# Kernel optimization log

Measured on AMD Instinct MI355X. Metric: run time of the kernel, lower is better.

Reference implementation:

```python
import jax, jax.numpy as jnp
import numpy as np

STRIDE = 1
PADDING = 1
DILATION = 1


def setup_inputs() -> dict:
    key = jax.random.key(0)
    k1, k2 = jax.random.split(key)
    N, C_in, H, W = 32, 128, 56, 56
    C_out, ksz = 256, 3
    x = jax.random.normal(k1, (N, C_in, H, W), dtype=jnp.float32)
    # xavier_normal_ with gain sqrt(2): std = gain*sqrt(2/(fan_in+fan_out))
    fan_in = C_in * ksz * ksz
    fan_out = C_out * ksz * ksz
    std = np.sqrt(2.0) * np.sqrt(2.0 / (fan_in + fan_out))
    weight = jax.random.normal(k2, (C_out, C_in, ksz, ksz), dtype=jnp.float32) * jnp.float32(std)
    bias = jnp.zeros((C_out,), dtype=jnp.float32)
    return {"x": x, "weight": weight, "bias": bias}


def reference(x, weight, bias):
    # Faithful to conv2d(X, K, stride, padding, dilation, bias):
    # unfold (im2col) + matmul + fold is mathematically a standard cross-correlation
    # conv; expressed here with the efficient lax primitive.
    y = jax.lax.conv_general_dilated(
        x, weight,
        window_strides=(STRIDE, STRIDE),
        padding=[(PADDING, PADDING), (PADDING, PADDING)],
        rhs_dilation=(DILATION, DILATION),
        dimension_numbers=("NCHW", "OIHW", "NCHW"),
    )
    return y + bias[None, :, None, None]
```

## Files before the change

kernel.cpp:

```cpp
#include <hip/hip_runtime.h>
#include <hip/hip_bf16.h>


#define CIN   128
#define HH    56
#define WW    56
#define COUT  256
#define HW    3136
#define NIMG  32
#define NP    (NIMG * HW)
#define XPW   58
#define XPIX  (XPW * XPW)
#define XPAD_BYTES (NIMG * XPIX * CIN * 2)
#define WT_OFF     XPAD_BYTES

typedef __bf16 bf16x8 __attribute__((ext_vector_type(8)));
typedef float  f32x4  __attribute__((ext_vector_type(4)));

#define GLD16(g, l) __builtin_amdgcn_global_load_lds( \
    (const __attribute__((address_space(1))) void*)(g), \
    (__attribute__((address_space(3))) void*)(l), 16, 0, 0)

__device__ __forceinline__ unsigned pack_bf16(float a, float b) {
    return (__float_as_uint(b) & 0xFFFF0000u) | (__float_as_uint(a) >> 16);
}

__global__ __launch_bounds__(128) void prep_x(const float* __restrict__ x,
                                              __hip_bfloat16* __restrict__ xp) {
    __shared__ unsigned short t[HH * CIN];
    const int b  = blockIdx.x;
    const int n  = b / HH;
    const int y  = b - n * HH;
    const int ci = threadIdx.x;

    const float* src = x + ((size_t)(n * CIN + ci) * HW) + y * WW;
    #pragma unroll
    for (int j = 0; j < 14; ++j) {
        const float4 v = ((const float4*)src)[j];
        t[(4 * j + 0) * CIN + ci] = (unsigned short)(__float_as_uint(v.x) >> 16);
        t[(4 * j + 1) * CIN + ci] = (unsigned short)(__float_as_uint(v.y) >> 16);
        t[(4 * j + 2) * CIN + ci] = (unsigned short)(__float_as_uint(v.z) >> 16);
        t[(4 * j + 3) * CIN + ci] = (unsigned short)(__float_as_uint(v.w) >> 16);
    }

    const uint4 z = make_uint4(0, 0, 0, 0);
    if (ci < 32) {
        const int side = ci >> 4;
        const int j    = ci & 15;
        ((uint4*)(xp + ((size_t)n * XPIX + (y + 1) * XPW + side * 57) * CIN))[j] = z;
    }
    if (y == 0)
        for (int j = ci; j < 928; j += 128)
            ((uint4*)(xp + (size_t)n * XPIX * CIN))[j] = z;
    if (y == HH - 1)
        for (int j = ci; j < 928; j += 128)
            ((uint4*)(xp + ((size_t)n * XPIX + 57 * XPW) * CIN))[j] = z;

    __syncthreads();

    uint4* dst = (uint4*)(xp + ((size_t)n * XPIX + (y + 1) * XPW + 1) * CIN);
    const uint4* lsrc = (const uint4*)t;
    #pragma unroll
    for (int j = 0; j < 7; ++j)
        dst[j * 128 + ci] = lsrc[j * 128 + ci];
}

__global__ __launch_bounds__(256) void prep_w(const float* __restrict__ w,
                                              __hip_bfloat16* __restrict__ wt) {
    const int co = blockIdx.x * 2 + (threadIdx.x >> 7);
    const int ci = threadIdx.x & 127;
    const float* src = w + (size_t)(co * CIN + ci) * 9;
    #pragma unroll
    for (int tp = 0; tp < 9; ++tp)
        wt[(size_t)tp * (COUT * CIN) + co * CIN + ci] = __float2bfloat16(src[tp]);
}

__global__ __launch_bounds__(256) void conv_main(
    const char* __restrict__ xpb,
    const char* __restrict__ wtb,
    const float* __restrict__ bias,
    float* __restrict__ out)
{
    __shared__ __align__(16) char L[65536];

    const int tid  = threadIdx.x;
    const int l    = tid & 63;
    const int wv   = tid >> 6;
    const int wm   = wv & 1;
    const int wn   = wv >> 1;
    const int l15  = l & 15;
    const int quad = l >> 4;

    const int idx = blockIdx.x;
    const int bm  = (idx >> 3) & 1;
    const int bn  = (idx >> 4) * 8 + (idx & 7);
    const int pbase  = bn * 128;
    const int cobase = bm * 128;

    const int gseg = (l & 3) ^ ((l >> 3) & 3);
    unsigned aoff[2], boff[2];
    #pragma unroll
    for (int j = 0; j < 2; ++j) {
        const int c   = wv * 2 + j;
        const int row = c * 16 + (l >> 2);
        aoff[j] = (unsigned)((cobase + row) * 256 + gseg * 16);
        const int p   = pbase + row;
        const int n   = p / HW;
        const int rem = p - n * HW;
        const int y   = rem / WW;
        const int x   = rem - y * WW;
        boff[j] = (unsigned)((n * XPIX + y * XPW + x) * 256 + gseg * 16);
    }
    const int segoff = (quad ^ ((l15 >> 1) & 3)) << 4;

    f32x4 acc[4][4];
    #pragma unroll
    for (int i = 0; i < 4; ++i)
        #pragma unroll
        for (int j = 0; j < 4; ++j)
            acc[i][j] = (f32x4){0.f, 0.f, 0.f, 0.f};

    auto STAGE = [&](int s, int bufw) {
        const int t  = s >> 2;
        const int kq = s & 3;
        const int r  = t / 3;
        const int sx = t - 3 * r;
        const unsigned wo = (unsigned)(t * (COUT * CIN * 2) + kq * 64);
        const unsigned bo = (unsigned)((r * XPW + sx) * 256 + kq * 64);
        char* Ab = L + bufw * 8192;
        char* Bb = L + 32768 + bufw * 8192;
        #pragma unroll
        for (int j = 0; j < 2; ++j) {
            const int c = wv * 2 + j;
            GLD16(wtb + wo + aoff[j], Ab + c * 1024);
            GLD16(xpb + bo + boff[j], Bb + c * 1024);
        }
    };

    STAGE(0, 0);
    STAGE(1, 1);
    STAGE(2, 2);

    #pragma unroll
    for (int s = 0; s < 36; ++s) {
        asm volatile("s_waitcnt vmcnt(8)" ::: "memory");
        __builtin_amdgcn_s_barrier();
        asm volatile("" ::: "memory");

        STAGE((s + 3 < 36) ? s + 3 : 35, (s + 3) & 3);

        const char* Ab = L + (s & 3) * 8192;
        const char* Bb = L + 32768 + (s & 3) * 8192;
        bf16x8 af[4], bfr[4];
        #pragma unroll
        for (int mt = 0; mt < 4; ++mt)
            af[mt] = *(const bf16x8*)(Ab + (wm * 64 + mt * 16 + l15) * 64 + segoff);
        #pragma unroll
        for (int nt = 0; nt < 4; ++nt)
            bfr[nt] = *(const bf16x8*)(Bb + (wn * 64 + nt * 16 + l15) * 64 + segoff);

        __builtin_amdgcn_s_setprio(1);
        #pragma unroll
        for (int mt = 0; mt < 4; ++mt)
            #pragma unroll
            for (int nt = 0; nt < 4; ++nt)
                acc[mt][nt] = __builtin_amdgcn_mfma_f32_16x16x32_bf16(
                    af[mt], bfr[nt], acc[mt][nt], 0, 0, 0);
        __builtin_amdgcn_s_setprio(0);
    }

    asm volatile("s_waitcnt vmcnt(0)" ::: "memory");

    #pragma unroll
    for (int nt = 0; nt < 4; ++nt) {
        const int pp = pbase + wn * 64 + nt * 16 + l15;
        const int n2 = pp / HW;
        const int r2 = pp - n2 * HW;
        float* ob = out + (size_t)n2 * (COUT * HW) + r2;
        #pragma unroll
        for (int mt = 0; mt < 4; ++mt) {
            const int co = cobase + wm * 64 + mt * 16 + quad * 4;
            const float4 bv = *(const float4*)(bias + co);
            f32x4 a = acc[mt][nt];
            ob[(size_t)(co + 0) * HW] = a[0] + bv.x;
            ob[(size_t)(co + 1) * HW] = a[1] + bv.y;
            ob[(size_t)(co + 2) * HW] = a[2] + bv.z;
            ob[(size_t)(co + 3) * HW] = a[3] + bv.w;
        }
    }
}

extern "C" void kernel_launch(void* const* d_in, const int* in_sizes, int n_in,
                              void* d_out, int out_size, void* d_ws, size_t ws_size,
                              hipStream_t stream) {
    const float* x = (const float*)d_in[0];
    const float* w = (const float*)d_in[1];
    const float* b = (const float*)d_in[2];
    char* ws = (char*)d_ws;
    __hip_bfloat16* xp = (__hip_bfloat16*)ws;
    __hip_bfloat16* wt = (__hip_bfloat16*)(ws + WT_OFF);

    prep_x<<<dim3(NIMG * HH), dim3(128), 0, stream>>>(x, xp);
    prep_w<<<dim3(128), dim3(256), 0, stream>>>(w, wt);
    conv_main<<<dim3((NP / 128) * 2), dim3(256), 0, stream>>>(
        (const char*)xp, (const char*)wt, b, (float*)d_out);
}
```

Before: 213.3 us.

## Widen conv tile to all 256 output channels with 8 waves and triple buffering

Each block now covers all 256 output channels for 128 pixels using 512 threads (8 waves), so every activation tile is loaded once instead of twice across two channel-half blocks. The LDS pipeline moves from 4 stages to 3 stages of 24KB. The block index mapping is remapped across 8 groups for locality. This halves the redundant B (input) traffic, at the cost of fewer blocks, a shallower prefetch depth and more LDS per block, which may limit occupancy.

```diff
diff --git a/kernel.cpp b/kernel.cpp
--- a/kernel.cpp
+++ b/kernel.cpp
@@ -21,10 +21,6 @@
     (const __attribute__((address_space(1))) void*)(g), \
     (__attribute__((address_space(3))) void*)(l), 16, 0, 0)
 
-__device__ __forceinline__ unsigned pack_bf16(float a, float b) {
-    return (__float_as_uint(b) & 0xFFFF0000u) | (__float_as_uint(a) >> 16);
-}
-
 __global__ __launch_bounds__(128) void prep_x(const float* __restrict__ x,
                                               __hip_bfloat16* __restrict__ xp) {
     __shared__ unsigned short t[HH * CIN];
@@ -75,41 +71,42 @@
         wt[(size_t)tp * (COUT * CIN) + co * CIN + ci] = __float2bfloat16(src[tp]);
 }
 
-__global__ __launch_bounds__(256) void conv_main(
+__global__ __launch_bounds__(512, 4) void conv_main(
     const char* __restrict__ xpb,
     const char* __restrict__ wtb,
     const float* __restrict__ bias,
     float* __restrict__ out)
 {
-    __shared__ __align__(16) char L[65536];
+    __shared__ __align__(16) char L[73728];
 
     const int tid  = threadIdx.x;
     const int l    = tid & 63;
     const int wv   = tid >> 6;
-    const int wm   = wv & 1;
-    const int wn   = wv >> 1;
+    const int wm   = wv >> 1;
+    const int wn   = wv & 1;
     const int l15  = l & 15;
     const int quad = l >> 4;
 
     const int idx = blockIdx.x;
-    const int bm  = (idx >> 3) & 1;
-    const int bn  = (idx >> 4) * 8 + (idx & 7);
-    const int pbase  = bn * 128;
-    const int cobase = bm * 128;
+    const int bn  = (idx & 7) * 98 + (idx >> 3);
+    const int pbase = bn * 128;
 
     const int gseg = (l & 3) ^ ((l >> 3) & 3);
-    unsigned aoff[2], boff[2];
+    unsigned aoff[2];
     #pragma unroll
     for (int j = 0; j < 2; ++j) {
-        const int c   = wv * 2 + j;
-        const int row = c * 16 + (l >> 2);
-        aoff[j] = (unsigned)((cobase + row) * 256 + gseg * 16);
-        const int p   = pbase + row;
+        const int rA = (wv * 2 + j) * 16 + (l >> 2);
+        aoff[j] = (unsigned)(rA * 256 + gseg * 16);
+    }
+    unsigned boff;
+    {
+        const int rB  = wv * 16 + (l >> 2);
+        const int p   = pbase + rB;
         const int n   = p / HW;
         const int rem = p - n * HW;
         const int y   = rem / WW;
         const int x   = rem - y * WW;
-        boff[j] = (unsigned)((n * XPIX + y * XPW + x) * 256 + gseg * 16);
+        boff = (unsigned)((n * XPIX + y * XPW + x) * 256 + gseg * 16);
     }
     const int segoff = (quad ^ ((l15 >> 1) & 3)) << 4;
 
@@ -121,43 +118,40 @@
             acc[i][j] = (f32x4){0.f, 0.f, 0.f, 0.f};
 
     auto STAGE = [&](int s, int bufw) {
-        const int t  = s >> 2;
+        const int tp = s >> 2;
         const int kq = s & 3;
-        const int r  = t / 3;
-        const int sx = t - 3 * r;
-        const unsigned wo = (unsigned)(t * (COUT * CIN * 2) + kq * 64);
+        const int r  = tp / 3;
+        const int sx = tp - 3 * r;
+        const unsigned wo = (unsigned)(tp * (COUT * CIN * 2) + kq * 64);
         const unsigned bo = (unsigned)((r * XPW + sx) * 256 + kq * 64);
-        char* Ab = L + bufw * 8192;
-        char* Bb = L + 32768 + bufw * 8192;
-        #pragma unroll
-        for (int j = 0; j < 2; ++j) {
-            const int c = wv * 2 + j;
-            GLD16(wtb + wo + aoff[j], Ab + c * 1024);
-            GLD16(xpb + bo + boff[j], Bb + c * 1024);
-        }
+        char* Ab = L + bufw * 24576;
+        char* Bb = Ab + 16384;
+        #pragma unroll
+        for (int j = 0; j < 2; ++j)
+            GLD16(wtb + wo + aoff[j], Ab + (wv * 2 + j) * 1024);
+        GLD16(xpb + bo + boff, Bb + wv * 1024);
     };
 
     STAGE(0, 0);
     STAGE(1, 1);
-    STAGE(2, 2);
-
-    #pragma unroll
-    for (int s = 0; s < 36; ++s) {
-        asm volatile("s_waitcnt vmcnt(8)" ::: "memory");
+
+    #pragma unroll
+    for (int t = 0; t < 36; ++t) {
+        asm volatile("s_waitcnt vmcnt(3)" ::: "memory");
         __builtin_amdgcn_s_barrier();
         asm volatile("" ::: "memory");
 
-        STAGE((s + 3 < 36) ? s + 3 : 35, (s + 3) & 3);
-
-        const char* Ab = L + (s & 3) * 8192;
-        const char* Bb = L + 32768 + (s & 3) * 8192;
-        bf16x8 af[4], bfr[4];
+        STAGE((t + 2 < 36) ? t + 2 : 35, (t + 2) % 3);
+
+        const char* Ab = L + (t % 3) * 24576;
+        const char* Bb = Ab + 16384;
+        bf16x8 af[4], bf[4];
         #pragma unroll
         for (int mt = 0; mt < 4; ++mt)
             af[mt] = *(const bf16x8*)(Ab + (wm * 64 + mt * 16 + l15) * 64 + segoff);
         #pragma unroll
         for (int nt = 0; nt < 4; ++nt)
-            bfr[nt] = *(const bf16x8*)(Bb + (wn * 64 + nt * 16 + l15) * 64 + segoff);
+            bf[nt] = *(const bf16x8*)(Bb + (wn * 64 + nt * 16 + l15) * 64 + segoff);
 
         __builtin_amdgcn_s_setprio(1);
         #pragma unroll
@@ -165,7 +159,7 @@
             #pragma unroll
             for (int nt = 0; nt < 4; ++nt)
                 acc[mt][nt] = __builtin_amdgcn_mfma_f32_16x16x32_bf16(
-                    af[mt], bfr[nt], acc[mt][nt], 0, 0, 0);
+                    af[mt], bf[nt], acc[mt][nt], 0, 0, 0);
         __builtin_amdgcn_s_setprio(0);
     }
 
@@ -179,7 +173,7 @@
         float* ob = out + (size_t)n2 * (COUT * HW) + r2;
         #pragma unroll
         for (int mt = 0; mt < 4; ++mt) {
-            const int co = cobase + wm * 64 + mt * 16 + quad * 4;
+            const int co = wm * 64 + mt * 16 + quad * 4;
             const float4 bv = *(const float4*)(bias + co);
             f32x4 a = acc[mt][nt];
             ob[(size_t)(co + 0) * HW] = a[0] + bv.x;
@@ -202,6 +196,6 @@
 
     prep_x<<<dim3(NIMG * HH), dim3(128), 0, stream>>>(x, xp);
     prep_w<<<dim3(128), dim3(256), 0, stream>>>(w, wt);
-    conv_main<<<dim3((NP / 128) * 2), dim3(256), 0, stream>>>(
+    conv_main<<<dim3(NP / 128), dim3(512), 0, stream>>>(
         (const char*)xp, (const char*)wt, b, (float*)d_out);
 }
```

Measured after the change: 216.6 us. No clear change (+1.5%).

## Load MFMA operands directly from global memory, dropping LDS staging pipeline

Applied to the files above, without the earlier changes.

Removes the 4-stage LDS ring buffer filled with global_load_lds, along with its barriers and priority hints. Each wave now loads its bf16 A and B fragments straight from global memory into registers every k-step. It also adds a launch-bounds occupancy hint of 4 blocks. This trades LDS traffic and block-wide syncs for redundant global/L2 reads, since each fragment is now fetched by two waves instead of shared, and loses explicit prefetch overlap.

```diff
diff --git a/kernel.cpp b/kernel.cpp
--- a/kernel.cpp
+++ b/kernel.cpp
@@ -16,14 +16,6 @@
 
 typedef __bf16 bf16x8 __attribute__((ext_vector_type(8)));
 typedef float  f32x4  __attribute__((ext_vector_type(4)));
-
-#define GLD16(g, l) __builtin_amdgcn_global_load_lds( \
-    (const __attribute__((address_space(1))) void*)(g), \
-    (__attribute__((address_space(3))) void*)(l), 16, 0, 0)
-
-__device__ __forceinline__ unsigned pack_bf16(float a, float b) {
-    return (__float_as_uint(b) & 0xFFFF0000u) | (__float_as_uint(a) >> 16);
-}
 
 __global__ __launch_bounds__(128) void prep_x(const float* __restrict__ x,
                                               __hip_bfloat16* __restrict__ xp) {
@@ -75,14 +67,12 @@
         wt[(size_t)tp * (COUT * CIN) + co * CIN + ci] = __float2bfloat16(src[tp]);
 }
 
-__global__ __launch_bounds__(256) void conv_main(
+__global__ __launch_bounds__(256, 4) void conv_main(
     const char* __restrict__ xpb,
     const char* __restrict__ wtb,
     const float* __restrict__ bias,
     float* __restrict__ out)
 {
-    __shared__ __align__(16) char L[65536];
-
     const int tid  = threadIdx.x;
     const int l    = tid & 63;
     const int wv   = tid >> 6;
@@ -97,21 +87,20 @@
     const int pbase  = bn * 128;
     const int cobase = bm * 128;
 
-    const int gseg = (l & 3) ^ ((l >> 3) & 3);
-    unsigned aoff[2], boff[2];
+    const char* ab[4];
     #pragma unroll
-    for (int j = 0; j < 2; ++j) {
-        const int c   = wv * 2 + j;
-        const int row = c * 16 + (l >> 2);
-        aoff[j] = (unsigned)((cobase + row) * 256 + gseg * 16);
-        const int p   = pbase + row;
+    for (int mt = 0; mt < 4; ++mt)
+        ab[mt] = wtb + (size_t)(cobase + wm * 64 + mt * 16 + l15) * 256 + quad * 16;
+    const char* bb[4];
+    #pragma unroll
+    for (int nt = 0; nt < 4; ++nt) {
+        const int p   = pbase + wn * 64 + nt * 16 + l15;
         const int n   = p / HW;
         const int rem = p - n * HW;
         const int y   = rem / WW;
         const int x   = rem - y * WW;
-        boff[j] = (unsigned)((n * XPIX + y * XPW + x) * 256 + gseg * 16);
+        bb[nt] = xpb + (size_t)(n * XPIX + y * XPW + x) * 256 + quad * 16;
     }
-    const int segoff = (quad ^ ((l15 >> 1) & 3)) << 4;
 
     f32x4 acc[4][4];
     #pragma unroll
@@ -120,56 +109,30 @@
         for (int j = 0; j < 4; ++j)
             acc[i][j] = (f32x4){0.f, 0.f, 0.f, 0.f};
 
-    auto STAGE = [&](int s, int bufw) {
-        const int t  = s >> 2;
-        const int kq = s & 3;
-        const int r  = t / 3;
-        const int sx = t - 3 * r;
-        const unsigned wo = (unsigned)(t * (COUT * CIN * 2) + kq * 64);
-        const unsigned bo = (unsigned)((r * XPW + sx) * 256 + kq * 64);
-        char* Ab = L + bufw * 8192;
-        char* Bb = L + 32768 + bufw * 8192;
-        #pragma unroll
-        for (int j = 0; j < 2; ++j) {
-            const int c = wv * 2 + j;
-            GLD16(wtb + wo + aoff[j], Ab + c * 1024);
-            GLD16(xpb + bo + boff[j], Bb + c * 1024);
-        }
-    };
-
-    STAGE(0, 0);
-    STAGE(1, 1);
-    STAGE(2, 2);
-
     #pragma unroll
     for (int s = 0; s < 36; ++s) {
-        asm volatile("s_waitcnt vmcnt(8)" ::: "memory");
-        __builtin_amdgcn_s_barrier();
-        asm volatile("" ::: "memory");
+        const int tp = s >> 2;
+        const int kq = s & 3;
+        const int r  = tp / 3;
+        const int sx = tp - 3 * r;
+        const unsigned wo = (unsigned)(tp * (COUT * CIN * 2) + kq * 64);
+        const unsigned bo = (unsigned)((r * XPW + sx) * 256 + kq * 64);
 
-        STAGE((s + 3 < 36) ? s + 3 : 35, (s + 3) & 3);
-
-        const char* Ab = L + (s & 3) * 8192;
-        const char* Bb = L + 32768 + (s & 3) * 8192;
-        bf16x8 af[4], bfr[4];
+        bf16x8 af[4], bf[4];
         #pragma unroll
         for (int mt = 0; mt < 4; ++mt)
-            af[mt] = *(const bf16x8*)(Ab + (wm * 64 + mt * 16 + l15) * 64 + segoff);
+            af[mt] = *(const bf16x8*)(ab[mt] + wo);
         #pragma unroll
         for (int nt = 0; nt < 4; ++nt)
-            bfr[nt] = *(const bf16x8*)(Bb + (wn * 64 + nt * 16 + l15) * 64 + segoff);
+            bf[nt] = *(const bf16x8*)(bb[nt] + bo);
 
-        __builtin_amdgcn_s_setprio(1);
         #pragma unroll
         for (int mt = 0; mt < 4; ++mt)
             #pragma unroll
             for (int nt = 0; nt < 4; ++nt)
                 acc[mt][nt] = __builtin_amdgcn_mfma_f32_16x16x32_bf16(
-                    af[mt], bfr[nt], acc[mt][nt], 0, 0, 0);
-        __builtin_amdgcn_s_setprio(0);
+                    af[mt], bf[nt], acc[mt][nt], 0, 0, 0);
     }
-
-    asm volatile("s_waitcnt vmcnt(0)" ::: "memory");
 
     #pragma unroll
     for (int nt = 0; nt < 4; ++nt) {
```

New measurement: 394.7 us. 85.1% more time.
